# Kernel optimization log

Measured on AMD Instinct MI355X. Metric: run time of the kernel, lower is better.

The kernel has to match this reference:

```python
import jax, jax.numpy as jnp
import numpy as np

N = 80000    # total nodes
E = 640000   # total edges
B = 800      # graphs in batch
NPG = 100    # nodes per graph
HID = 128
NC = 10
IND = 20     # one-hot degree feature size (torch.eye(20))
EPS = 1e-5


def _gconv(x, src, dst, inv_out, inv_in, W, b):
    # DGL GraphConv, norm='both': D_out^{-1/2} scaling at src, sum-aggregate, D_in^{-1/2} at dst
    m = (x * inv_out[:, None])[src]                      # [E, F]
    agg = jax.ops.segment_sum(m, dst, num_segments=x.shape[0])
    return (agg * inv_in[:, None]) @ W + b


def _bn(x, gamma, beta):
    # BatchNorm1d, training-mode (batch statistics, biased variance)
    mu = x.mean(0)
    var = x.var(0)
    return (x - mu) / jnp.sqrt(var + EPS) * gamma + beta


def setup_inputs():
    key = jax.random.key(0)
    ks = jax.random.split(key, 10)
    # edges constrained within each graph (batched disjoint graphs, as in dgl.batch)
    eg = jax.random.randint(ks[0], (E,), 0, B)
    src = (eg * NPG + jax.random.randint(ks[1], (E,), 0, NPG)).astype(jnp.int32)
    dst = (eg * NPG + jax.random.randint(ks[2], (E,), 0, NPG)).astype(jnp.int32)
    graph_id = (jnp.arange(N) // NPG).astype(jnp.int32)

    def p(k, shape, fan):
        return (jax.random.normal(k, shape, jnp.float32) / np.sqrt(fan)).astype(jnp.float32)

    z = lambda s: jnp.zeros(s, jnp.float32)
    o = lambda s: jnp.ones(s, jnp.float32)
    return dict(
        src=src, dst=dst, graph_id=graph_id,
        W1=p(ks[3], (IND, HID), IND), b1=z((HID,)), g1=o((HID,)), be1=z((HID,)),
        W2=p(ks[4], (HID, HID), HID), b2=z((HID,)), g2=o((HID,)), be2=z((HID,)),
        Wv=p(ks[5], (HID, 1), HID), bv=z((1,)),
        Wd=p(ks[6], (1, HID), 1), bd=z((HID,)),
        Wg=p(ks[7], (HID, HID), HID), bg=z((HID,)), g3=o((HID,)), be3=z((HID,)),
        Wc=p(ks[8], (HID, NC), HID), bc=z((NC,)),
    )


def reference(src, dst, graph_id, W1, b1, g1, be1, W2, b2, g2, be2,
              Wv, bv, Wd, bd, Wg, bg, g3, be3, Wc, bc):
    n = graph_id.shape[0]
    ones_e = jnp.ones(src.shape[0], jnp.float32)
    in_deg = jax.ops.segment_sum(ones_e, dst, num_segments=n)
    out_deg = jax.ops.segment_sum(ones_e, src, num_segments=n)
    inv_in = jax.lax.rsqrt(jnp.maximum(in_deg, 1.0))   # DGL clamps deg min 1
    inv_out = jax.lax.rsqrt(jnp.maximum(out_deg, 1.0))

    # node features: one-hot of in-degree (eye(20)[in_degrees]); clip to valid range
    h = jax.nn.one_hot(jnp.clip(in_deg.astype(jnp.int32), 0, IND - 1), IND, dtype=jnp.float32)
    h = jax.nn.elu(_bn(_gconv(h, src, dst, inv_out, inv_in, W1, b1), g1, be1))  # [N,HID]
    h = jax.nn.elu(_bn(_gconv(h, src, dst, inv_out, inv_in, W2, b2), g2, be2))  # [N,HID]

    v = _gconv(h, src, dst, inv_out, inv_in, Wv, bv)   # [N,1], node weights d
    d = v[:, 0]

    # per-graph ragged matmul: vec_i = d_i^T @ h_i, done as one segment-sum
    vec = jax.ops.segment_sum(d[:, None] * h, graph_id, num_segments=B).reshape(-1)  # [B*HID]
    mean = vec.mean()
    vec = jax.nn.relu(vec - mean) - jax.nn.relu(-vec - mean)   # soft shrink by global mean

    hg = jnp.tanh(vec.reshape(B, HID))
    hg = jnp.tanh(_bn(hg @ Wg + bg, g3, be3))
    return jnp.tanh(hg @ Wc + bc)   # [B, NC] (eval-mode output)
```

## Files before the change

### kernel.cpp

```cpp
#include <hip/hip_runtime.h>
#include <hip/hip_bf16.h>
#include <math.h>

#define N_NODES 80000
#define N_EDGES 640000
#define B_GR 800
#define NPG 100
#define HID 128
#define NC 10
#define IND 20
#define BN_EPS 1e-5f
#define ENT_CAP 1024

__global__ void k_A(const int* __restrict__ src, const int* __restrict__ dst,
                    unsigned int* A) {
    int e = blockIdx.x * blockDim.x + threadIdx.x;
    if (e < N_EDGES) {
        int s = src[e], d = dst[e];
        int g = d / NPG;
        int bidx = g * (NPG * NPG) + (d - g * NPG) * NPG + (s - g * NPG);
        atomicAdd(&A[bidx >> 2], 1u << ((bidx & 3) * 8));
    }
}

__global__ __launch_bounds__(128) void k_prep(const unsigned int* __restrict__ A,
                                              float* __restrict__ inv_in,
                                              float* __restrict__ inv_out,
                                              float* __restrict__ agg20,
                                              unsigned int* __restrict__ ent,
                                              int* __restrict__ goff) {
    __shared__ unsigned int s_A[NPG * 25];
    __shared__ float s_io[NPG];
    __shared__ int   s_ix[NPG];
    __shared__ float s_agg[NPG][IND + 1];
    __shared__ int s_offs[128];
    int g = blockIdx.x, gbase = g * NPG, t = threadIdx.x;
    const unsigned int* Ag = A + g * 2500;
    for (int i = t; i < NPG * 25; i += 128) s_A[i] = Ag[i];
    __syncthreads();

    int nnz = 0;
    if (t < NPG) {
        int rsum = 0;
        const unsigned int* row = &s_A[t * 25];
#pragma unroll
        for (int q = 0; q < 25; ++q) {
            unsigned int c4 = row[q];
            rsum += (int)((c4 & 255u) + ((c4 >> 8) & 255u) + ((c4 >> 16) & 255u) + (c4 >> 24));
            nnz += (int)((c4 & 255u) != 0) + (int)(((c4 >> 8) & 255u) != 0)
                 + (int)(((c4 >> 16) & 255u) != 0) + (int)((c4 >> 24) != 0);
        }
        int csum = 0;
        int wq = t >> 2, sh = (t & 3) * 8;
#pragma unroll 4
        for (int r = 0; r < NPG; ++r)
            csum += (int)((s_A[r * 25 + wq] >> sh) & 255u);

        float io = rsqrtf(fmaxf((float)csum, 1.f));
        inv_in[gbase + t]  = rsqrtf(fmaxf((float)rsum, 1.f));
        inv_out[gbase + t] = io;
        s_io[t] = io;
        s_ix[t] = rsum > IND - 1 ? IND - 1 : rsum;
    }
    int v = nnz;
    s_offs[t] = v;
    __syncthreads();
    for (int d = 1; d < 128; d <<= 1) {
        int x = (t >= d) ? s_offs[t - d] : 0;
        __syncthreads();
        s_offs[t] += x;
        __syncthreads();
    }
    int my_off = s_offs[t] - v;
    if (t < NPG) goff[g * 104 + t] = my_off;
    if (t == 0) goff[g * 104 + NPG] = s_offs[127];
    __syncthreads();

    if (t < NPG) {
#pragma unroll
        for (int k = 0; k < IND; ++k) s_agg[t][k] = 0.f;
        const unsigned int* row = &s_A[t * 25];
        unsigned int* ep = ent + (size_t)g * ENT_CAP + my_off;
        int w = 0;
#pragma unroll
        for (int q = 0; q < 25; ++q) {
            unsigned int c4 = row[q];
            if (c4 == 0) continue;
#pragma unroll
            for (int b = 0; b < 4; ++b) {
                unsigned int cnt = (c4 >> (8 * b)) & 255u;
                if (cnt) {
                    int s = q * 4 + b;
                    s_agg[t][s_ix[s]] += (float)cnt * s_io[s];
                    ep[w++] = ((unsigned int)s << 8) | cnt;
                }
            }
        }
        float* outp = agg20 + (size_t)(gbase + t) * IND;
#pragma unroll
        for (int k = 0; k < IND; ++k) outp[k] = s_agg[t][k];
    }
}

#define MOM_CHUNK 64
__global__ __launch_bounds__(256) void k_mom(const float* __restrict__ agg20,
                                             const float* __restrict__ inv_in,
                                             float* s20, float* Mbuf) {
    __shared__ float rows[MOM_CHUNK * IND];
    __shared__ float w1s[MOM_CHUNK], w2s[MOM_CHUNK];
    int t = threadIdx.x;
    int k = 0, l = 0;
    bool isM = (t < 210), isS = (t >= 210 && t < 230);
    if (isM) {
        int idx = t, kk = 0;
        while (idx >= IND - kk) { idx -= IND - kk; ++kk; }
        k = kk; l = kk + idx;
    } else if (isS) {
        k = t - 210;
    }
    float acc = 0.f;
    for (int c = blockIdx.x; c < N_NODES / MOM_CHUNK; c += gridDim.x) {
        __syncthreads();
        for (int i = t * 4; i < MOM_CHUNK * IND; i += 1024)
            *(float4*)&rows[i] = *(const float4*)&agg20[(size_t)c * MOM_CHUNK * IND + i];
        if (t < MOM_CHUNK) {
            float v = inv_in[c * MOM_CHUNK + t];
            w1s[t] = v; w2s[t] = v * v;
        }
        __syncthreads();
        if (isM) {
            for (int i = 0; i < MOM_CHUNK; ++i)
                acc += w2s[i] * rows[i * IND + k] * rows[i * IND + l];
        } else if (isS) {
            for (int i = 0; i < MOM_CHUNK; ++i)
                acc += w1s[i] * rows[i * IND + k];
        }
    }
    if (isM) atomicAdd(&Mbuf[t], acc);
    else if (isS) atomicAdd(&s20[t - 210], acc);
}

__global__ void k_bn1fin(const float* __restrict__ s20, const float* __restrict__ Mbuf,
                         const float* __restrict__ W1, const float* __restrict__ b1,
                         const float* __restrict__ g1, const float* __restrict__ be1,
                         float* a1, float* c1) {
    __shared__ float sM[210], ss[IND];
    int j = threadIdx.x;
    if (j < 210) sM[j] = Mbuf[j];
    if (j + 128 < 210) sM[j + 128] = Mbuf[j + 128];
    if (j < IND) ss[j] = s20[j];
    __syncthreads();
    float w[IND];
#pragma unroll
    for (int k = 0; k < IND; ++k) w[k] = W1[k * HID + j];
    float tj = 0.f;
#pragma unroll
    for (int k = 0; k < IND; ++k) tj += ss[k] * w[k];
    float q = 0.f;
    int idx = 0;
#pragma unroll
    for (int k = 0; k < IND; ++k) {
        q += sM[idx] * w[k] * w[k]; ++idx;
#pragma unroll
        for (int l = k + 1; l < IND; ++l) { q += 2.f * sM[idx] * w[k] * w[l]; ++idx; }
    }
    float bj = b1[j];
    const float Nf = (float)N_NODES;
    float mean = (tj + Nf * bj) / Nf;
    float ey2  = (q + 2.f * bj * tj + Nf * bj * bj) / Nf;
    float var  = ey2 - mean * mean;
    float aj = g1[j] / sqrtf(var + BN_EPS);
    a1[j] = aj;
    c1[j] = be1[j] - mean * aj;
}

__global__ __launch_bounds__(256) void k_l1f(const float* __restrict__ agg20,
                                             const float* __restrict__ inv_in,
                                             const float* __restrict__ inv_out,
                                             const float* __restrict__ W1,
                                             const float* __restrict__ b1,
                                             const float* __restrict__ a1,
                                             const float* __restrict__ c1,
                                             float* __restrict__ h1s) {
    __shared__ float ws[IND * HID];
    int t = threadIdx.x;
    for (int i = t * 4; i < IND * HID; i += 1024)
        *(float4*)&ws[i] = *(const float4*)&W1[i];
    __syncthreads();
    int tx = t & 15, ty = t >> 4;
    int c0 = tx * 8;
    float4 ba = *(const float4*)(b1 + c0);
    float4 bb = *(const float4*)(b1 + c0 + 4);
    float4 aa = *(const float4*)(a1 + c0);
    float4 ab = *(const float4*)(a1 + c0 + 4);
    float4 ca = *(const float4*)(c1 + c0);
    float4 cb = *(const float4*)(c1 + c0 + 4);

    int row0 = blockIdx.x * 64 + ty * 4;
    const float* xr0 = agg20 + (size_t)row0 * IND;
    const float* xr1 = xr0 + IND;
    const float* xr2 = xr1 + IND;
    const float* xr3 = xr2 + IND;
    float acc[4][8];
#pragma unroll
    for (int r = 0; r < 4; ++r)
#pragma unroll
        for (int c = 0; c < 8; ++c) acc[r][c] = 0.f;

#pragma unroll
    for (int k = 0; k < IND; k += 4) {
        float4 x0 = *(const float4*)(xr0 + k);
        float4 x1 = *(const float4*)(xr1 + k);
        float4 x2 = *(const float4*)(xr2 + k);
        float4 x3 = *(const float4*)(xr3 + k);
#pragma unroll
        for (int kk = 0; kk < 4; ++kk) {
            float4 wa = *(const float4*)&ws[(k + kk) * HID + c0];
            float4 wb = *(const float4*)&ws[(k + kk) * HID + c0 + 4];
            float xk0 = (kk == 0) ? x0.x : (kk == 1) ? x0.y : (kk == 2) ? x0.z : x0.w;
            float xk1 = (kk == 0) ? x1.x : (kk == 1) ? x1.y : (kk == 2) ? x1.z : x1.w;
            float xk2 = (kk == 0) ? x2.x : (kk == 1) ? x2.y : (kk == 2) ? x2.z : x2.w;
            float xk3 = (kk == 0) ? x3.x : (kk == 1) ? x3.y : (kk == 2) ? x3.z : x3.w;
            acc[0][0] += xk0 * wa.x; acc[0][1] += xk0 * wa.y;
            acc[0][2] += xk0 * wa.z; acc[0][3] += xk0 * wa.w;
            acc[0][4] += xk0 * wb.x; acc[0][5] += xk0 * wb.y;
            acc[0][6] += xk0 * wb.z; acc[0][7] += xk0 * wb.w;
            acc[1][0] += xk1 * wa.x; acc[1][1] += xk1 * wa.y;
            acc[1][2] += xk1 * wa.z; acc[1][3] += xk1 * wa.w;
            acc[1][4] += xk1 * wb.x; acc[1][5] += xk1 * wb.y;
            acc[1][6] += xk1 * wb.z; acc[1][7] += xk1 * wb.w;
            acc[2][0] += xk2 * wa.x; acc[2][1] += xk2 * wa.y;
            acc[2][2] += xk2 * wa.z; acc[2][3] += xk2 * wa.w;
            acc[2][4] += xk2 * wb.x; acc[2][5] += xk2 * wb.y;
            acc[2][6] += xk2 * wb.z; acc[2][7] += xk2 * wb.w;
            acc[3][0] += xk3 * wa.x; acc[3][1] += xk3 * wa.y;
            acc[3][2] += xk3 * wa.z; acc[3][3] += xk3 * wa.w;
            acc[3][4] += xk3 * wb.x; acc[3][5] += xk3 * wb.y;
            acc[3][6] += xk3 * wb.z; acc[3][7] += xk3 * wb.w;
        }
    }
    float4 iv = *(const float4*)(inv_in + row0);
    float4 ov = *(const float4*)(inv_out + row0);
#pragma unroll
    for (int r = 0; r < 4; ++r) {
        float ivr = (r == 0) ? iv.x : (r == 1) ? iv.y : (r == 2) ? iv.z : iv.w;
        float ovr = (r == 0) ? ov.x : (r == 1) ? ov.y : (r == 2) ? ov.z : ov.w;
        float y[8];
        y[0] = acc[r][0] * ivr + ba.x; y[1] = acc[r][1] * ivr + ba.y;
        y[2] = acc[r][2] * ivr + ba.z; y[3] = acc[r][3] * ivr + ba.w;
        y[4] = acc[r][4] * ivr + bb.x; y[5] = acc[r][5] * ivr + bb.y;
        y[6] = acc[r][6] * ivr + bb.z; y[7] = acc[r][7] * ivr + bb.w;
        float z[8];
        z[0] = y[0] * aa.x + ca.x; z[1] = y[1] * aa.y + ca.y;
        z[2] = y[2] * aa.z + ca.z; z[3] = y[3] * aa.w + ca.w;
        z[4] = y[4] * ab.x + cb.x; z[5] = y[5] * ab.y + cb.y;
        z[6] = y[6] * ab.z + cb.z; z[7] = y[7] * ab.w + cb.w;
#pragma unroll
        for (int c = 0; c < 8; ++c) {
            float h = z[c] > 0.f ? z[c] : expm1f(z[c]);
            z[c] = h * ovr;
        }
        float* yr = h1s + (size_t)(row0 + r) * HID + c0;
        *(float4*)yr = make_float4(z[0], z[1], z[2], z[3]);
        *(float4*)(yr + 4) = make_float4(z[4], z[5], z[6], z[7]);
    }
}

__global__ __launch_bounds__(512) void k_agg2v6(const unsigned int* __restrict__ ent,
                                                const int* __restrict__ goff,
                                                const float* __restrict__ h1s,
                                                float* __restrict__ agg2) {
    __shared__ float sh[NPG * HID];
    __shared__ int s_off[NPG + 1];
    int t = threadIdx.x;
    int g = blockIdx.x;
    int gbase = g * NPG;

    const float4* srcp = (const float4*)(h1s + (size_t)gbase * HID);
    float4* shp = (float4*)sh;
    for (int i = t; i < (NPG * HID) / 4; i += 512)
        shp[i] = srcp[i];
    if (t <= NPG) s_off[t] = goff[g * 104 + t];
    __syncthreads();

    int wv = t >> 6, lane = t & 63;
    const unsigned int* ep = ent + (size_t)g * ENT_CAP;
    for (int r = wv; r < NPG; r += 8) {
        int e0 = s_off[r], e1 = s_off[r + 1];
        float ax = 0.f, ay = 0.f;
        int i = e0;
        for (; i + 8 <= e1; i += 8) {
            unsigned int ee[8];
#pragma unroll
            for (int j = 0; j < 8; ++j) ee[j] = ep[i + j];
#pragma unroll
            for (int j = 0; j < 8; ++j) {
                float f = (float)(ee[j] & 255u);
                int s = ee[j] >> 8;
                float2 v = *(const float2*)&sh[s * HID + lane * 2];
                ax += f * v.x; ay += f * v.y;
            }
        }
        for (; i < e1; ++i) {
            unsigned int e = ep[i];
            float f = (float)(e & 255u);
            int s = e >> 8;
            float2 v = *(const float2*)&sh[s * HID + lane * 2];
            ax += f * v.x; ay += f * v.y;
        }
        *(float2*)(agg2 + (size_t)(gbase + r) * HID + lane * 2) = make_float2(ax, ay);
    }
}

__global__ void k_bnfin(const float* sums, const float* sqs,
                        const float* gamma, const float* beta,
                        float cnt, float* a, float* c) {
    int j = threadIdx.x;
    float mu  = sums[j] / cnt;
    float var = sqs[j] / cnt - mu * mu;
    float aj  = gamma[j] / sqrtf(var + BN_EPS);
    a[j] = aj;
    c[j] = beta[j] - mu * aj;
}

__global__ __launch_bounds__(512) void k_l2v5(const float* __restrict__ xin,
                                              const float* __restrict__ inv_in,
                                              const float* __restrict__ W,
                                              const float* __restrict__ bvec,
                                              float* __restrict__ yout,
                                              float* sums, float* sqs) {
    __shared__ float ws[HID * 64];
    int t = threadIdx.x;
    int tile = blockIdx.x >> 1;
    int half = blockIdx.x & 1;
    int cbase = half * 64;
    for (int i = t; i < HID * 16; i += 512) {
        int k = i >> 4;
        int c4 = (i & 15) << 2;
        *(float4*)&ws[k * 64 + c4] = *(const float4*)&W[k * HID + cbase + c4];
    }
    __syncthreads();

    int tx = t & 15;
    int ty = t >> 4;
    int c0 = tx * 4;
    float4 ba = *(const float4*)(bvec + cbase + c0);
    float csum[4], csq[4];
#pragma unroll
    for (int c = 0; c < 4; ++c) { csum[c] = 0.f; csq[c] = 0.f; }

    int row0 = tile * 128 + ty * 4;
    const float* xr0 = xin + (size_t)row0 * HID;
    const float* xr1 = xr0 + HID;
    const float* xr2 = xr1 + HID;
    const float* xr3 = xr2 + HID;
    float acc[4][4];
#pragma unroll
    for (int r = 0; r < 4; ++r)
#pragma unroll
        for (int c = 0; c < 4; ++c) acc[r][c] = 0.f;

#pragma unroll 4
    for (int k = 0; k < HID; k += 4) {
        float4 x0 = *(const float4*)(xr0 + k);
        float4 x1 = *(const float4*)(xr1 + k);
        float4 x2 = *(const float4*)(xr2 + k);
        float4 x3 = *(const float4*)(xr3 + k);
#pragma unroll
        for (int kk = 0; kk < 4; ++kk) {
            float4 wa = *(const float4*)&ws[(k + kk) * 64 + c0];
            float xk0 = (kk == 0) ? x0.x : (kk == 1) ? x0.y : (kk == 2) ? x0.z : x0.w;
            float xk1 = (kk == 0) ? x1.x : (kk == 1) ? x1.y : (kk == 2) ? x1.z : x1.w;
            float xk2 = (kk == 0) ? x2.x : (kk == 1) ? x2.y : (kk == 2) ? x2.z : x2.w;
            float xk3 = (kk == 0) ? x3.x : (kk == 1) ? x3.y : (kk == 2) ? x3.z : x3.w;
            acc[0][0] += xk0 * wa.x; acc[0][1] += xk0 * wa.y;
            acc[0][2] += xk0 * wa.z; acc[0][3] += xk0 * wa.w;
            acc[1][0] += xk1 * wa.x; acc[1][1] += xk1 * wa.y;
            acc[1][2] += xk1 * wa.z; acc[1][3] += xk1 * wa.w;
            acc[2][0] += xk2 * wa.x; acc[2][1] += xk2 * wa.y;
            acc[2][2] += xk2 * wa.z; acc[2][3] += xk2 * wa.w;
            acc[3][0] += xk3 * wa.x; acc[3][1] += xk3 * wa.y;
            acc[3][2] += xk3 * wa.z; acc[3][3] += xk3 * wa.w;
        }
    }
    float4 iv = *(const float4*)(inv_in + row0);
#pragma unroll
    for (int r = 0; r < 4; ++r) {
        float ivr = (r == 0) ? iv.x : (r == 1) ? iv.y : (r == 2) ? iv.z : iv.w;
        float y0 = acc[r][0] * ivr + ba.x;
        float y1 = acc[r][1] * ivr + ba.y;
        float y2 = acc[r][2] * ivr + ba.z;
        float y3 = acc[r][3] * ivr + ba.w;
        csum[0] += y0; csq[0] += y0 * y0;
        csum[1] += y1; csq[1] += y1 * y1;
        csum[2] += y2; csq[2] += y2 * y2;
        csum[3] += y3; csq[3] += y3 * y3;
        *(float4*)(yout + (size_t)(row0 + r) * HID + cbase + c0) = make_float4(y0, y1, y2, y3);
    }

    __syncthreads();
#pragma unroll
    for (int c = 0; c < 4; ++c) {
        ws[ty * 64 + c0 + c] = csum[c];
        ws[2048 + ty * 64 + c0 + c] = csq[c];
    }
    __syncthreads();
    if (t < 64) {
        float s1 = 0.f, s2 = 0.f;
#pragma unroll
        for (int r = 0; r < 32; ++r) {
            s1 += ws[r * 64 + t];
            s2 += ws[2048 + r * 64 + t];
        }
        atomicAdd(&sums[cbase + t], s1);
        atomicAdd(&sqs[cbase + t], s2);
    }
}

__global__ __launch_bounds__(512) void k_post(const unsigned int* __restrict__ ent,
                                              const int* __restrict__ goff,
                                              const float* __restrict__ y2,
                                              const float* __restrict__ a2,
                                              const float* __restrict__ c2,
                                              const float* __restrict__ inv_in,
                                              const float* __restrict__ inv_out,
                                              const float* __restrict__ Wv,
                                              const float* __restrict__ bv,
                                              float* __restrict__ vec,
                                              float* meansum) {
    __shared__ float sh[NPG * HID];
    __shared__ float s_p[NPG];
    __shared__ float s_d[NPG];
    __shared__ float s_red[512];
    __shared__ int s_off[NPG + 1];
    int t = threadIdx.x;
    int g = blockIdx.x, gbase = g * NPG;

    const float4* srcp = (const float4*)(y2 + (size_t)gbase * HID);
    for (int i = t; i < (NPG * HID) / 4; i += 512) {
        int col = (i * 4) & (HID - 1);
        float4 v = srcp[i];
        float4 av = *(const float4*)(a2 + col);
        float4 cv = *(const float4*)(c2 + col);
        float z0 = v.x * av.x + cv.x; z0 = z0 > 0.f ? z0 : expm1f(z0);
        float z1 = v.y * av.y + cv.y; z1 = z1 > 0.f ? z1 : expm1f(z1);
        float z2 = v.z * av.z + cv.z; z2 = z2 > 0.f ? z2 : expm1f(z2);
        float z3 = v.w * av.w + cv.w; z3 = z3 > 0.f ? z3 : expm1f(z3);
        *(float4*)&sh[i * 4] = make_float4(z0, z1, z2, z3);
    }
    if (t <= NPG) s_off[t] = goff[g * 104 + t];
    __syncthreads();

    int wv = t >> 6, lane = t & 63;
    float2 wvv = *(const float2*)(Wv + lane * 2);
    for (int r = wv; r < NPG; r += 8) {
        float2 h = *(const float2*)&sh[r * HID + lane * 2];
        float d = h.x * wvv.x + h.y * wvv.y;
        for (int off = 32; off; off >>= 1) d += __shfl_down(d, off);
        if (lane == 0) s_p[r] = d * inv_out[gbase + r];
    }
    __syncthreads();

    if (t < NPG) {
        const unsigned int* ep = ent + (size_t)g * ENT_CAP;
        int e0 = s_off[t], e1 = s_off[t + 1];
        float acc = 0.f;
        for (int i = e0; i < e1; ++i) {
            unsigned int e = ep[i];
            acc += (float)(e & 255u) * s_p[e >> 8];
        }
        s_d[t] = acc * inv_in[gbase + t] + bv[0];
    }
    __syncthreads();

    int col = t & (HID - 1);
    int qr = t >> 7;
    float part = 0.f;
    for (int r = qr * 25; r < qr * 25 + 25; ++r)
        part += s_d[r] * sh[r * HID + col];
    s_red[qr * HID + col] = part;
    __syncthreads();
    if (t < HID) {
        float v = s_red[t] + s_red[HID + t] + s_red[2 * HID + t] + s_red[3 * HID + t];
        vec[g * HID + t] = v;
        for (int off = 32; off; off >>= 1) v += __shfl_down(v, off);
        if ((t & 63) == 0) atomicAdd(meansum, v);
    }
}

__global__ __launch_bounds__(128) void k_g1(const float* __restrict__ vec,
                                            const float* __restrict__ meansum,
                                            const float* __restrict__ Wg,
                                            const float* __restrict__ bg,
                                            float* y3, float* sums, float* sqs) {
    __shared__ float ws[HID * HID];
    __shared__ float rows[HID];
    int g = blockIdx.x, j = threadIdx.x;
    for (int k = 0; k < HID; ++k) ws[k * HID + j] = Wg[k * HID + j];
    float mean = meansum[0] * (1.f / (B_GR * HID));
    float v = vec[g * HID + j];
    float sh = fmaxf(v - mean, 0.f) - fmaxf(-v - mean, 0.f);
    rows[j] = tanhf(sh);
    __syncthreads();
    float acc = 0.f;
#pragma unroll 8
    for (int k = 0; k < HID; ++k) acc += rows[k] * ws[k * HID + j];
    float y = acc + bg[j];
    y3[g * HID + j] = y;
    atomicAdd(&sums[j], y);
    atomicAdd(&sqs[j], y * y);
}

__global__ __launch_bounds__(128) void k_out(const float* __restrict__ y3,
                                             const float* __restrict__ a,
                                             const float* __restrict__ c,
                                             const float* __restrict__ Wc,
                                             const float* __restrict__ bc,
                                             float* out) {
    __shared__ float hg[HID];
    int g = blockIdx.x, j = threadIdx.x;
    hg[j] = tanhf(y3[g * HID + j] * a[j] + c[j]);
    __syncthreads();
    if (j < NC) {
        float acc = 0.f;
        for (int k = 0; k < HID; ++k) acc += hg[k] * Wc[k * NC + j];
        out[g * NC + j] = tanhf(acc + bc[j]);
    }
}

extern "C" void kernel_launch(void* const* d_in, const int* in_sizes, int n_in,
                              void* d_out, int out_size, void* d_ws, size_t ws_size,
                              hipStream_t stream) {
    const int*   src = (const int*)d_in[0];
    const int*   dst = (const int*)d_in[1];
    const float* W1  = (const float*)d_in[3];
    const float* b1  = (const float*)d_in[4];
    const float* g1  = (const float*)d_in[5];
    const float* be1 = (const float*)d_in[6];
    const float* W2  = (const float*)d_in[7];
    const float* b2  = (const float*)d_in[8];
    const float* g2  = (const float*)d_in[9];
    const float* be2 = (const float*)d_in[10];
    const float* Wv  = (const float*)d_in[11];
    const float* bv  = (const float*)d_in[12];
    const float* Wg  = (const float*)d_in[15];
    const float* bg  = (const float*)d_in[16];
    const float* g3  = (const float*)d_in[17];
    const float* be3 = (const float*)d_in[18];
    const float* Wc  = (const float*)d_in[19];
    const float* bc  = (const float*)d_in[20];
    float* out = (float*)d_out;

    char* ws = (char*)d_ws;
    size_t off = 0;
    auto carve = [&](size_t bytes) -> char* {
        char* pp = ws + off;
        off = (off + bytes + 255) & ~(size_t)255;
        return pp;
    };
    unsigned int* A = (unsigned int*)carve((size_t)B_GR * NPG * NPG);
    float* stats   = (float*)carve(2048 * 4);
    size_t zbytes = off;
    float* inv_in  = (float*)carve(N_NODES * 4);
    float* inv_out = (float*)carve(N_NODES * 4);
    float* vec     = (float*)carve((size_t)B_GR * HID * 4);
    float* y3      = (float*)carve((size_t)B_GR * HID * 4);
    float* agg20   = (float*)carve((size_t)N_NODES * IND * 4);
    float* bufA    = (float*)carve((size_t)N_NODES * HID * 4);
    float* bufB    = (float*)carve((size_t)N_NODES * HID * 4);
    unsigned int* ent = (unsigned int*)carve((size_t)B_GR * ENT_CAP * 4);
    int* goff      = (int*)carve((size_t)B_GR * 104 * 4);

    float* sums2 = stats + 0;    float* sq2 = stats + 128;
    float* a2    = stats + 256;  float* c2  = stats + 384;
    float* sums3 = stats + 512;  float* sq3 = stats + 640;
    float* a3    = stats + 768;  float* c3  = stats + 896;
    float* meansum = stats + 1024;
    float* s20   = stats + 1056;
    float* Mbuf  = stats + 1088;
    float* a1    = stats + 1312;
    float* c1    = stats + 1440;

    hipMemsetAsync(d_ws, 0, zbytes, stream);

    k_A<<<(N_EDGES + 255) / 256, 256, 0, stream>>>(src, dst, A);
    k_prep<<<B_GR, 128, 0, stream>>>(A, inv_in, inv_out, agg20, ent, goff);
    k_mom<<<320, 256, 0, stream>>>(agg20, inv_in, s20, Mbuf);
    k_bn1fin<<<1, 128, 0, stream>>>(s20, Mbuf, W1, b1, g1, be1, a1, c1);
    k_l1f<<<N_NODES / 64, 256, 0, stream>>>(agg20, inv_in, inv_out, W1, b1, a1, c1, bufA);
    k_agg2v6<<<B_GR, 512, 0, stream>>>(ent, goff, bufA, bufB);
    k_l2v5<<<(N_NODES / 128) * 2, 512, 0, stream>>>(bufB, inv_in, W2, b2, bufA, sums2, sq2);
    k_bnfin<<<1, 128, 0, stream>>>(sums2, sq2, g2, be2, (float)N_NODES, a2, c2);
    k_post<<<B_GR, 512, 0, stream>>>(ent, goff, bufA, a2, c2, inv_in, inv_out, Wv, bv,
                                     vec, meansum);
    k_g1<<<B_GR, 128, 0, stream>>>(vec, meansum, Wg, bg, y3, sums3, sq3);
    k_bnfin<<<1, 128, 0, stream>>>(sums3, sq3, g3, be3, (float)B_GR, a3, c3);
    k_out<<<B_GR, 128, 0, stream>>>(y3, a3, c3, Wc, bc, out);
}
```

Baseline: 270.0 us.

## Fuse layer-2 aggregation with W2 GEMM and BN statistics per graph

Merges the per-graph neighbour aggregation kernel and the separate layer-2 GEMM kernel into one kernel. Aggregated rows stay in registers, are written back into shared memory, and each block then multiplies its 100 rows by W2, applies the inv_in scale and bias, and accumulates BatchNorm sums. This removes one launch and the global round trip of the 80000x128 intermediate. In exchange the GEMM reads W2 from global memory with scalar loads per k, keeps 25 accumulators per thread, and has low arithmetic reuse per block, so register pressure and GEMM efficiency may be worse than the dedicated tiled kernel.

Measured after the change: 283.8 us. 5.1% more time.

```diff
diff --git a/kernel.cpp b/kernel.cpp
--- a/kernel.cpp
+++ b/kernel.cpp
@@ -266,15 +266,18 @@
     }
 }
 
-__global__ __launch_bounds__(512) void k_agg2v6(const unsigned int* __restrict__ ent,
+__global__ __launch_bounds__(512) void k_aggemm(const unsigned int* __restrict__ ent,
                                                 const int* __restrict__ goff,
                                                 const float* __restrict__ h1s,
-                                                float* __restrict__ agg2) {
+                                                const float* __restrict__ inv_in,
+                                                const float* __restrict__ W2,
+                                                const float* __restrict__ b2,
+                                                float* __restrict__ y2,
+                                                float* sums, float* sqs) {
     __shared__ float sh[NPG * HID];
     __shared__ int s_off[NPG + 1];
     int t = threadIdx.x;
-    int g = blockIdx.x;
-    int gbase = g * NPG;
+    int g = blockIdx.x, gbase = g * NPG;
 
     const float4* srcp = (const float4*)(h1s + (size_t)gbase * HID);
     float4* shp = (float4*)sh;
@@ -285,30 +288,82 @@
 
     int wv = t >> 6, lane = t & 63;
     const unsigned int* ep = ent + (size_t)g * ENT_CAP;
-    for (int r = wv; r < NPG; r += 8) {
-        int e0 = s_off[r], e1 = s_off[r + 1];
+    float2 ar[13];
+#pragma unroll
+    for (int i = 0; i < 13; ++i) {
+        int r = wv + 8 * i;
         float ax = 0.f, ay = 0.f;
-        int i = e0;
-        for (; i + 8 <= e1; i += 8) {
-            unsigned int ee[8];
-#pragma unroll
-            for (int j = 0; j < 8; ++j) ee[j] = ep[i + j];
-#pragma unroll
-            for (int j = 0; j < 8; ++j) {
-                float f = (float)(ee[j] & 255u);
-                int s = ee[j] >> 8;
+        if (r < NPG) {
+            int e0 = s_off[r], e1 = s_off[r + 1];
+            int e = e0;
+            for (; e + 8 <= e1; e += 8) {
+                unsigned int ee[8];
+#pragma unroll
+                for (int j = 0; j < 8; ++j) ee[j] = ep[e + j];
+#pragma unroll
+                for (int j = 0; j < 8; ++j) {
+                    float f = (float)(ee[j] & 255u);
+                    int s = ee[j] >> 8;
+                    float2 v = *(const float2*)&sh[s * HID + lane * 2];
+                    ax += f * v.x; ay += f * v.y;
+                }
+            }
+            for (; e < e1; ++e) {
+                unsigned int eo = ep[e];
+                float f = (float)(eo & 255u);
+                int s = eo >> 8;
                 float2 v = *(const float2*)&sh[s * HID + lane * 2];
                 ax += f * v.x; ay += f * v.y;
             }
         }
-        for (; i < e1; ++i) {
-            unsigned int e = ep[i];
-            float f = (float)(e & 255u);
-            int s = e >> 8;
-            float2 v = *(const float2*)&sh[s * HID + lane * 2];
-            ax += f * v.x; ay += f * v.y;
-        }
-        *(float2*)(agg2 + (size_t)(gbase + r) * HID + lane * 2) = make_float2(ax, ay);
+        ar[i] = make_float2(ax, ay);
+    }
+    __syncthreads();
+
+#pragma unroll
+    for (int i = 0; i < 13; ++i) {
+        int r = wv + 8 * i;
+        if (r < NPG)
+            *(float2*)&sh[r * HID + lane * 2] = ar[i];
+    }
+    __syncthreads();
+
+    int tx = t & 127, ty = t >> 7;
+    int rbase = ty * 25;
+    float acc[25];
+#pragma unroll
+    for (int r = 0; r < 25; ++r) acc[r] = 0.f;
+    for (int k = 0; k < HID; k += 4) {
+        float w0 = W2[(k + 0) * HID + tx];
+        float w1 = W2[(k + 1) * HID + tx];
+        float w2v = W2[(k + 2) * HID + tx];
+        float w3 = W2[(k + 3) * HID + tx];
+#pragma unroll
+        for (int r = 0; r < 25; ++r) {
+            float4 a = *(const float4*)&sh[(rbase + r) * HID + k];
+            acc[r] += a.x * w0 + a.y * w1 + a.z * w2v + a.w * w3;
+        }
+    }
+
+    float bj = b2[tx];
+    float cs = 0.f, cq = 0.f;
+#pragma unroll
+    for (int r = 0; r < 25; ++r) {
+        int row = gbase + rbase + r;
+        float y = acc[r] * inv_in[row] + bj;
+        y2[(size_t)row * HID + tx] = y;
+        cs += y; cq += y * y;
+    }
+
+    __syncthreads();
+    sh[ty * HID + tx] = cs;
+    sh[512 + ty * HID + tx] = cq;
+    __syncthreads();
+    if (t < HID) {
+        float s = sh[t] + sh[HID + t] + sh[2 * HID + t] + sh[3 * HID + t];
+        float q = sh[512 + t] + sh[512 + HID + t] + sh[512 + 2 * HID + t] + sh[512 + 3 * HID + t];
+        atomicAdd(&sums[t], s);
+        atomicAdd(&sqs[t], q);
     }
 }
 
@@ -321,100 +376,6 @@
     float aj  = gamma[j] / sqrtf(var + BN_EPS);
     a[j] = aj;
     c[j] = beta[j] - mu * aj;
-}
-
-__global__ __launch_bounds__(512) void k_l2v5(const float* __restrict__ xin,
-                                              const float* __restrict__ inv_in,
-                                              const float* __restrict__ W,
-                                              const float* __restrict__ bvec,
-                                              float* __restrict__ yout,
-                                              float* sums, float* sqs) {
-    __shared__ float ws[HID * 64];
-    int t = threadIdx.x;
-    int tile = blockIdx.x >> 1;
-    int half = blockIdx.x & 1;
-    int cbase = half * 64;
-    for (int i = t; i < HID * 16; i += 512) {
-        int k = i >> 4;
-        int c4 = (i & 15) << 2;
-        *(float4*)&ws[k * 64 + c4] = *(const float4*)&W[k * HID + cbase + c4];
-    }
-    __syncthreads();
-
-    int tx = t & 15;
-    int ty = t >> 4;
-    int c0 = tx * 4;
-    float4 ba = *(const float4*)(bvec + cbase + c0);
-    float csum[4], csq[4];
-#pragma unroll
-    for (int c = 0; c < 4; ++c) { csum[c] = 0.f; csq[c] = 0.f; }
-
-    int row0 = tile * 128 + ty * 4;
-    const float* xr0 = xin + (size_t)row0 * HID;
-    const float* xr1 = xr0 + HID;
-    const float* xr2 = xr1 + HID;
-    const float* xr3 = xr2 + HID;
-    float acc[4][4];
-#pragma unroll
-    for (int r = 0; r < 4; ++r)
-#pragma unroll
-        for (int c = 0; c < 4; ++c) acc[r][c] = 0.f;
-
-#pragma unroll 4
-    for (int k = 0; k < HID; k += 4) {
-        float4 x0 = *(const float4*)(xr0 + k);
-        float4 x1 = *(const float4*)(xr1 + k);
-        float4 x2 = *(const float4*)(xr2 + k);
-        float4 x3 = *(const float4*)(xr3 + k);
-#pragma unroll
-        for (int kk = 0; kk < 4; ++kk) {
-            float4 wa = *(const float4*)&ws[(k + kk) * 64 + c0];
-            float xk0 = (kk == 0) ? x0.x : (kk == 1) ? x0.y : (kk == 2) ? x0.z : x0.w;
-            float xk1 = (kk == 0) ? x1.x : (kk == 1) ? x1.y : (kk == 2) ? x1.z : x1.w;
-            float xk2 = (kk == 0) ? x2.x : (kk == 1) ? x2.y : (kk == 2) ? x2.z : x2.w;
-            float xk3 = (kk == 0) ? x3.x : (kk == 1) ? x3.y : (kk == 2) ? x3.z : x3.w;
-            acc[0][0] += xk0 * wa.x; acc[0][1] += xk0 * wa.y;
-            acc[0][2] += xk0 * wa.z; acc[0][3] += xk0 * wa.w;
-            acc[1][0] += xk1 * wa.x; acc[1][1] += xk1 * wa.y;
-            acc[1][2] += xk1 * wa.z; acc[1][3] += xk1 * wa.w;
-            acc[2][0] += xk2 * wa.x; acc[2][1] += xk2 * wa.y;
-            acc[2][2] += xk2 * wa.z; acc[2][3] += xk2 * wa.w;
-            acc[3][0] += xk3 * wa.x; acc[3][1] += xk3 * wa.y;
-            acc[3][2] += xk3 * wa.z; acc[3][3] += xk3 * wa.w;
-        }
-    }
-    float4 iv = *(const float4*)(inv_in + row0);
-#pragma unroll
-    for (int r = 0; r < 4; ++r) {
-        float ivr = (r == 0) ? iv.x : (r == 1) ? iv.y : (r == 2) ? iv.z : iv.w;
-        float y0 = acc[r][0] * ivr + ba.x;
-        float y1 = acc[r][1] * ivr + ba.y;
-        float y2 = acc[r][2] * ivr + ba.z;
-        float y3 = acc[r][3] * ivr + ba.w;
-        csum[0] += y0; csq[0] += y0 * y0;
-        csum[1] += y1; csq[1] += y1 * y1;
-        csum[2] += y2; csq[2] += y2 * y2;
-        csum[3] += y3; csq[3] += y3 * y3;
-        *(float4*)(yout + (size_t)(row0 + r) * HID + cbase + c0) = make_float4(y0, y1, y2, y3);
-    }
-
-    __syncthreads();
-#pragma unroll
-    for (int c = 0; c < 4; ++c) {
-        ws[ty * 64 + c0 + c] = csum[c];
-        ws[2048 + ty * 64 + c0 + c] = csq[c];
-    }
-    __syncthreads();
-    if (t < 64) {
-        float s1 = 0.f, s2 = 0.f;
-#pragma unroll
-        for (int r = 0; r < 32; ++r) {
-            s1 += ws[r * 64 + t];
-            s2 += ws[2048 + r * 64 + t];
-        }
-        atomicAdd(&sums[cbase + t], s1);
-        atomicAdd(&sqs[cbase + t], s2);
-    }
 }
 
 __global__ __launch_bounds__(512) void k_post(const unsigned int* __restrict__ ent,
@@ -588,10 +549,9 @@
     k_mom<<<320, 256, 0, stream>>>(agg20, inv_in, s20, Mbuf);
     k_bn1fin<<<1, 128, 0, stream>>>(s20, Mbuf, W1, b1, g1, be1, a1, c1);
     k_l1f<<<N_NODES / 64, 256, 0, stream>>>(agg20, inv_in, inv_out, W1, b1, a1, c1, bufA);
-    k_agg2v6<<<B_GR, 512, 0, stream>>>(ent, goff, bufA, bufB);
-    k_l2v5<<<(N_NODES / 128) * 2, 512, 0, stream>>>(bufB, inv_in, W2, b2, bufA, sums2, sq2);
+    k_aggemm<<<B_GR, 512, 0, stream>>>(ent, goff, bufA, inv_in, W2, b2, bufB, sums2, sq2);
     k_bnfin<<<1, 128, 0, stream>>>(sums2, sq2, g2, be2, (float)N_NODES, a2, c2);
-    k_post<<<B_GR, 512, 0, stream>>>(ent, goff, bufA, a2, c2, inv_in, inv_out, Wv, bv,
+    k_post<<<B_GR, 512, 0, stream>>>(ent, goff, bufB, a2, c2, inv_in, inv_out, Wv, bv,
                                      vec, meansum);
     k_g1<<<B_GR, 128, 0, stream>>>(vec, meansum, Wg, bg, y3, sums3, sq3);
     k_bnfin<<<1, 128, 0, stream>>>(sums3, sq3, g3, be3, (float)B_GR, a3, c3);
```
